# Optimization experiments

Measured on AMD Instinct MI355X. Metric: run time of the kernel, lower is better.

The kernel has to match this reference:

```python
import jax, jax.numpy as jnp
import numpy as np

B, T, I, H, O = 32, 128, 256, 512, 10


def setup_inputs() -> dict:
    key = jax.random.key(0)
    ks = jax.random.split(key, 16)
    s = 1.0 / np.sqrt(H)
    si = 1.0 / np.sqrt(I)
    inp = {
        "x": jax.random.normal(ks[0], (B, T, I), jnp.float32),
        # LSTM params (gate order: i, f, g, o)
        "Wih": jax.random.uniform(ks[1], (4 * H, I), jnp.float32, -si, si),
        "Whh": jax.random.uniform(ks[2], (4 * H, H), jnp.float32, -s, s),
        "b_lstm": jax.random.uniform(ks[3], (4 * H,), jnp.float32, -s, s),
        # readout dense
        "Wd": jax.random.uniform(ks[4], (O, H), jnp.float32, -s, s),
        "bd": jnp.zeros((O,), jnp.float32),
        # synthetic gradient MLP: H -> 512 -> 256 -> 128 -> H
        "Ws1": jax.random.uniform(ks[5], (512, H), jnp.float32, -s, s),
        "bs1": jnp.zeros((512,), jnp.float32),
        "Ws2": jax.random.uniform(ks[6], (256, 512), jnp.float32, -1.0 / np.sqrt(512), 1.0 / np.sqrt(512)),
        "bs2": jnp.zeros((256,), jnp.float32),
        "Ws3": jax.random.uniform(ks[7], (128, 256), jnp.float32, -1.0 / np.sqrt(256), 1.0 / np.sqrt(256)),
        "bs3": jnp.zeros((128,), jnp.float32),
        "Ws4": jax.random.uniform(ks[8], (H, 128), jnp.float32, -1.0 / np.sqrt(128), 1.0 / np.sqrt(128)),
        "bs4": jnp.zeros((H,), jnp.float32),
    }
    return inp


def reference(x, Wih, Whh, b_lstm, Wd, bd, Ws1, bs1, Ws2, bs2, Ws3, bs3, Ws4, bs4):
    # batch_first: [B,T,I] -> [T,B,I]
    xs = jnp.swapaxes(x, 0, 1)
    b, hid = x.shape[0], Whh.shape[1]

    h0 = jnp.zeros((b, hid), x.dtype)
    c0 = jnp.zeros((b, hid), x.dtype)
    # e-prop eligibility vectors: one row per (gate in {i,f,g}) x hidden unit
    ev_x0 = jnp.zeros((b, 3 * hid, Wih.shape[1]), x.dtype)
    ev_h0 = jnp.zeros((b, 3 * hid, hid), x.dtype)
    ev_b0 = jnp.zeros((b, 3 * hid, 1), x.dtype)

    def step(carry, xt):
        h, c, ev_x, ev_h, ev_b = carry
        gates = xt @ Wih.T + h @ Whh.T + b_lstm  # [B,4H]
        gi, gf, gg, go = jnp.split(gates, 4, axis=1)
        i = jax.nn.sigmoid(gi)
        f = jax.nn.sigmoid(gf)
        g = jnp.tanh(gg)
        o = jax.nn.sigmoid(go)
        # d(c_t)/d(pre-activation) for cell-affecting gates i, f, g  -> [B,3H]
        d = jnp.concatenate([g * i * (1.0 - i),
                             c * f * (1.0 - f),
                             i * (1.0 - g * g)], axis=1)
        f3 = jnp.concatenate([f, f, f], axis=1)  # forget-gate decay, tiled per gate
        # eligibility trace outer-product updates (the memory-bound core)
        ev_x_n = ev_x * f3[:, :, None] + d[:, :, None] * xt[:, None, :]
        ev_h_n = ev_h * f3[:, :, None] + d[:, :, None] * h[:, None, :]
        ev_b_n = ev_b * f3[:, :, None] + d[:, :, None]
        c_n = f * c + i * g
        h_n = o * jnp.tanh(c_n)
        return (h_n, c_n, ev_x_n, ev_h_n, ev_b_n), h_n

    (hT, cT, ev_x, ev_h, ev_b), hs = jax.lax.scan(step, (h0, c0, ev_x0, ev_h0, ev_b0), xs)

    last = hs[-1]  # [B,H]
    # synthetic gradient MLP on last hidden state
    z = jax.nn.relu(last @ Ws1.T + bs1)
    z = jax.nn.relu(z @ Ws2.T + bs2)
    z = jax.nn.relu(z @ Ws3.T + bs3)
    synth_grad = z @ Ws4.T + bs4  # [B,H]
    # readout on last hidden state (single_output=True)
    predictions = last @ Wd.T + bd  # [B,O]
    return (predictions, synth_grad, ev_x, ev_h, ev_b)
```

## Files before the change

kernel.cpp:

```cpp
#include <hip/hip_runtime.h>


typedef __attribute__((ext_vector_type(8))) short short8;
typedef __attribute__((ext_vector_type(4))) float f32x4;
typedef __attribute__((ext_vector_type(4))) unsigned u32x4;

#define DEV static __device__ __forceinline__

DEV unsigned f2bf(float x) {
  union { float f; unsigned u; } v; v.f = x;
  return (v.u + 0x7fffu + ((v.u >> 16) & 1u)) >> 16;
}
DEV float bf2f(unsigned b) {
  union { float f; unsigned u; } v; v.u = b << 16;
  return v.f;
}
struct HiLo { unsigned hi, lo; };
DEV HiLo packpair(float a, float b) {
  unsigned ha = f2bf(a), hb = f2bf(b);
  unsigned la = f2bf(a - bf2f(ha)), lb = f2bf(b - bf2f(hb));
  HiLo r; r.hi = ha | (hb << 16); r.lo = la | (lb << 16);
  return r;
}

#define SENT 0x7F7F7F7Fu

__global__ __launch_bounds__(512, 1) void lstm_rec(
    const float* __restrict__ Whh,
    const float* __restrict__ XW,
    unsigned* __restrict__ Hp,
    float* __restrict__ Hf,
    float* __restrict__ dh,
    float* __restrict__ fh)
{
  const int wg   = blockIdx.x;
  const int tid  = threadIdx.x;
  const int lane = tid & 63;
  const int wave = tid >> 6;
  const int tM   = wave & 1;
  const int tN   = wave >> 1;

  __shared__ __align__(16) unsigned Ldh[32 * 256];
  __shared__ float gl[32][68];

  const int cc = lane & 15;
  const int kb = lane >> 4;

  const int rloc  = tN * 16 + cc;
  const int jglob = (rloc >> 4) * 512 + wg * 16 + (rloc & 15);
  short8 whi[16], wlo[16];
#pragma unroll
  for (int s = 0; s < 16; ++s) {
    const float* wp = Whh + (size_t)jglob * 512 + s * 32 + kb * 8;
    f32x4 w0 = *(const f32x4*)wp;
    f32x4 w1 = *(const f32x4*)(wp + 4);
    short8 hi, lo;
#pragma unroll
    for (int j = 0; j < 4; ++j) {
      unsigned h0 = f2bf(w0[j]);
      hi[j] = (short)h0;  lo[j] = (short)f2bf(w0[j] - bf2f(h0));
      unsigned h1 = f2bf(w1[j]);
      hi[4 + j] = (short)h1;  lo[4 + j] = (short)f2bf(w1[j] - bf2f(h1));
    }
    whi[s] = hi; wlo[s] = lo;
  }

  const int bA = tM * 16 + cc;
  const int mz = bA & 7;
  const unsigned rbase = (unsigned)(bA * 256 + ((kb ^ (mz & 3)) << 2) + ((mz >> 2) << 4));

  const int beW = lane >> 1;
  const int swz = beW & 7;

  const int be = tid >> 4;
  const int jo = tid & 15;
  const int jh = wg * 16 + jo;
  float c_reg = 0.f;

  for (int t = 0; t < 128; ++t) {
    const float* xwp = XW + (size_t)t * 65536 + (size_t)be * 2048 + wg * 16 + jo;
    float xwi = xwp[0], xwf = xwp[512], xwg = xwp[1024], xwo = xwp[1536];

    if (t > 0) {
      const unsigned* sp = Hp + ((size_t)t * 32 + wave * 4) * 256 + lane * 4;
      u32x4 h0, h1, h2, h3;
      for (;;) {
#define SLICE_LOAD(dst, addr)                                          \
        asm volatile("global_load_dwordx4 %0, %1, off sc0 sc1"         \
                     : "=&v"(dst) : "v"(addr) : "memory")
        SLICE_LOAD(h0, sp);
        SLICE_LOAD(h1, sp + 256);
        SLICE_LOAD(h2, sp + 512);
        SLICE_LOAD(h3, sp + 768);
#undef SLICE_LOAD
        asm volatile("s_waitcnt vmcnt(0)" ::: "memory");
        __builtin_amdgcn_sched_barrier(0);
        unsigned bad = 0u;
#define CHK(v) bad |= (unsigned)((v[0] == SENT) | (v[1] == SENT) | \
                                 (v[2] == SENT) | (v[3] == SENT))
        CHK(h0); CHK(h1); CHK(h2); CHK(h3);
#undef CHK
        if (!__any((int)bad)) break;
        __builtin_amdgcn_s_sleep(1);
      }
      __builtin_amdgcn_sched_barrier(0);

      const int c0 = wave * 8 + (lane & 1);
      const unsigned wb = (unsigned)(beW * 256);
      *(u32x4*)&Ldh[wb + (((c0 + 0) ^ swz) << 2)] = h0;
      *(u32x4*)&Ldh[wb + (((c0 + 2) ^ swz) << 2)] = h1;
      *(u32x4*)&Ldh[wb + (((c0 + 4) ^ swz) << 2)] = h2;
      *(u32x4*)&Ldh[wb + (((c0 + 6) ^ swz) << 2)] = h3;
    }
    __syncthreads();

    f32x4 acc;
    {
      f32x4 a0 = {0.f, 0.f, 0.f, 0.f}, a1 = a0;
      if (t > 0) {
#pragma unroll
        for (int s = 0; s < 16; ++s) {
          const unsigned idx = rbase ^ (unsigned)(s << 4);
          short8 ah = __builtin_bit_cast(short8, *(const u32x4*)&Ldh[idx]);
          a0 = __builtin_amdgcn_mfma_f32_16x16x32_bf16(ah, whi[s], a0, 0, 0, 0);
          a1 = __builtin_amdgcn_mfma_f32_16x16x32_bf16(ah, wlo[s], a1, 0, 0, 0);
        }
      }
      acc = a0 + a1;
    }
#pragma unroll
    for (int r = 0; r < 4; ++r)
      gl[tM * 16 + kb * 4 + r][tN * 16 + cc] = acc[r];
    __syncthreads();

    {
      float pi = xwi + gl[be][jo];
      float pf = xwf + gl[be][16 + jo];
      float pg = xwg + gl[be][32 + jo];
      float po = xwo + gl[be][48 + jo];
      float ig = 1.f / (1.f + expf(-pi));
      float fg = 1.f / (1.f + expf(-pf));
      float gg = tanhf(pg);
      float og = 1.f / (1.f + expf(-po));
      float di = gg * ig * (1.f - ig);
      float df = c_reg * fg * (1.f - fg);
      float dg = ig * (1.f - gg * gg);
      c_reg = fg * c_reg + ig * gg;
      float hn = og * tanhf(c_reg);

      unsigned hh = f2bf(hn);
      unsigned hh_nb = (unsigned)__shfl_xor((int)hh, 1);
      if (!(tid & 1)) {
        unsigned stv = hh | (hh_nb << 16);
        size_t sa = ((size_t)(t + 1) * 32 + wg) * 256 + (tid >> 1);
        __hip_atomic_store(&Hp[sa], stv, __ATOMIC_RELAXED, __HIP_MEMORY_SCOPE_AGENT);
      }

      Hf[(size_t)(t + 1) * 16384 + (size_t)be * 512 + jh] = hn;
      size_t db = (size_t)t * 49152 + (size_t)be * 1536 + jh;
      dh[db] = di; dh[db + 512] = df; dh[db + 1024] = dg;
      fh[(size_t)t * 16384 + (size_t)be * 512 + jh] = fg;
    }
  }
}

__global__ __launch_bounds__(256) void suffix_pre(
    const float* __restrict__ fh, float* __restrict__ Cp)
{
  const int g = blockIdx.x * 256 + threadIdx.x;
  const int k = g >> 14, bjh = g & 16383;
  const int b = bjh >> 9, jh = bjh & 511;
  float P = 1.f;
  for (int t = k * 32; t < k * 32 + 32; ++t)
    P *= fh[(size_t)t * 16384 + (size_t)b * 512 + jh];
  Cp[g] = P;
}

__global__ __launch_bounds__(256) void suffix_main(
    float* __restrict__ dh, const float* __restrict__ fh,
    const float* __restrict__ Cp, float* __restrict__ Sp)
{
  const int g = blockIdx.x * 256 + threadIdx.x;
  const int k = g >> 14, bjh = g & 16383;
  const int b = bjh >> 9, jh = bjh & 511;
  float F = 1.f;
  for (int k2 = k + 1; k2 < 4; ++k2) F *= Cp[(k2 << 14) | bjh];
  float s0 = 0.f, s1 = 0.f, s2 = 0.f;
  for (int t = k * 32 + 31; t >= k * 32; --t) {
    size_t db = (size_t)t * 49152 + (size_t)b * 1536 + jh;
    float a0 = dh[db] * F, a1 = dh[db + 512] * F, a2 = dh[db + 1024] * F;
    dh[db] = a0; dh[db + 512] = a1; dh[db + 1024] = a2;
    s0 += a0; s1 += a1; s2 += a2;
    F *= fh[(size_t)t * 16384 + (size_t)b * 512 + jh];
  }
  size_t sb = (size_t)(k * 32 + b) * 1536 + jh;
  Sp[sb] = s0; Sp[sb + 512] = s1; Sp[sb + 1024] = s2;
}

__global__ __launch_bounds__(256) void evb_reduce(
    const float* __restrict__ Sp, float* __restrict__ evb)
{
  const int g = blockIdx.x * 256 + threadIdx.x;
  evb[g] = Sp[g] + Sp[49152 + g] + Sp[98304 + g] + Sp[147456 + g];
}

__global__ __launch_bounds__(256, 2) void gemm_bf16s(
    const float* __restrict__ A, const float* __restrict__ B,
    float* __restrict__ C, const float* __restrict__ bias,
    int M, int N, int K,
    long long sAm, long long sAk, long long aBatch,
    long long sBn, long long sBk, long long bBatch,
    long long sCm1, long long sCm2, int M1, long long cBatch)
{
  __shared__ __align__(16) unsigned Ahi[128 * 20], Alo[128 * 20];
  __shared__ __align__(16) unsigned Bhi[128 * 20], Blo[128 * 20];

  const int tid  = threadIdx.x;
  const int lane = tid & 63;
  const int wave = tid >> 6;
  const int wm   = wave >> 1;
  const int wn   = wave & 1;
  const int cc   = lane & 15;
  const int kb   = lane >> 4;
  const long long z = blockIdx.z;
  const float* Ab = A + z * aBatch;
  const float* Bb = B + z * bBatch;
  const int m0 = blockIdx.y * 128, n0 = blockIdx.x * 128;

  f32x4 acc[4][4];
#pragma unroll
  for (int i = 0; i < 4; ++i)
#pragma unroll
    for (int j = 0; j < 4; ++j) acc[i][j] = (f32x4){0.f, 0.f, 0.f, 0.f};

  for (int k0 = 0; k0 < K; k0 += 32) {
    if (sAk == 1) {
      const int r = tid >> 1, half = tid & 1;
      const float* s = Ab + (long long)(m0 + r) * sAm + (k0 + half * 16);
      f32x4 v0 = *(const f32x4*)s;
      f32x4 v1 = *(const f32x4*)(s + 4);
      f32x4 v2 = *(const f32x4*)(s + 8);
      f32x4 v3 = *(const f32x4*)(s + 12);
      u32x4 h0, h1, l0, l1;
      HiLo p;
      p = packpair(v0[0], v0[1]); h0[0] = p.hi; l0[0] = p.lo;
      p = packpair(v0[2], v0[3]); h0[1] = p.hi; l0[1] = p.lo;
      p = packpair(v1[0], v1[1]); h0[2] = p.hi; l0[2] = p.lo;
      p = packpair(v1[2], v1[3]); h0[3] = p.hi; l0[3] = p.lo;
      p = packpair(v2[0], v2[1]); h1[0] = p.hi; l1[0] = p.lo;
      p = packpair(v2[2], v2[3]); h1[1] = p.hi; l1[1] = p.lo;
      p = packpair(v3[0], v3[1]); h1[2] = p.hi; l1[2] = p.lo;
      p = packpair(v3[2], v3[3]); h1[3] = p.hi; l1[3] = p.lo;
      const int o = r * 20 + half * 8;
      *(u32x4*)&Ahi[o] = h0;  *(u32x4*)&Ahi[o + 4] = h1;
      *(u32x4*)&Alo[o] = l0;  *(u32x4*)&Alo[o + 4] = l1;
    } else {
#pragma unroll
      for (int it = 0; it < 2; ++it) {
        const int kp = tid >> 4;
        const int mr = (tid & 15) * 4 + it * 64;
        const float* s0 = Ab + (long long)(k0 + 2 * kp) * sAk + (m0 + mr);
        f32x4 va = *(const f32x4*)s0;
        f32x4 vb = *(const f32x4*)(s0 + sAk);
#pragma unroll
        for (int q = 0; q < 4; ++q) {
          HiLo p = packpair(va[q], vb[q]);
          Ahi[(mr + q) * 20 + kp] = p.hi;
          Alo[(mr + q) * 20 + kp] = p.lo;
        }
      }
    }
    if (sBk == 1) {
      const int r = tid >> 1, half = tid & 1;
      const float* s = Bb + (long long)(n0 + r) * sBn + (k0 + half * 16);
      f32x4 v0 = *(const f32x4*)s;
      f32x4 v1 = *(const f32x4*)(s + 4);
      f32x4 v2 = *(const f32x4*)(s + 8);
      f32x4 v3 = *(const f32x4*)(s + 12);
      u32x4 h0, h1, l0, l1;
      HiLo p;
      p = packpair(v0[0], v0[1]); h0[0] = p.hi; l0[0] = p.lo;
      p = packpair(v0[2], v0[3]); h0[1] = p.hi; l0[1] = p.lo;
      p = packpair(v1[0], v1[1]); h0[2] = p.hi; l0[2] = p.lo;
      p = packpair(v1[2], v1[3]); h0[3] = p.hi; l0[3] = p.lo;
      p = packpair(v2[0], v2[1]); h1[0] = p.hi; l1[0] = p.lo;
      p = packpair(v2[2], v2[3]); h1[1] = p.hi; l1[1] = p.lo;
      p = packpair(v3[0], v3[1]); h1[2] = p.hi; l1[2] = p.lo;
      p = packpair(v3[2], v3[3]); h1[3] = p.hi; l1[3] = p.lo;
      const int o = r * 20 + half * 8;
      *(u32x4*)&Bhi[o] = h0;  *(u32x4*)&Bhi[o + 4] = h1;
      *(u32x4*)&Blo[o] = l0;  *(u32x4*)&Blo[o + 4] = l1;
    } else {
#pragma unroll
      for (int it = 0; it < 2; ++it) {
        const int kp = tid >> 4;
        const int nr = (tid & 15) * 4 + it * 64;
        const float* s0 = Bb + (long long)(k0 + 2 * kp) * sBk + (n0 + nr);
        f32x4 va = *(const f32x4*)s0;
        f32x4 vb = *(const f32x4*)(s0 + sBk);
#pragma unroll
        for (int q = 0; q < 4; ++q) {
          HiLo p = packpair(va[q], vb[q]);
          Bhi[(nr + q) * 20 + kp] = p.hi;
          Blo[(nr + q) * 20 + kp] = p.lo;
        }
      }
    }
    __syncthreads();

    short8 ah[4], al[4], bh[4], bl[4];
#pragma unroll
    for (int mi = 0; mi < 4; ++mi) {
      const int row = wm * 64 + mi * 16 + cc;
      ah[mi] = __builtin_bit_cast(short8, *(const u32x4*)&Ahi[row * 20 + kb * 4]);
      al[mi] = __builtin_bit_cast(short8, *(const u32x4*)&Alo[row * 20 + kb * 4]);
    }
#pragma unroll
    for (int ni = 0; ni < 4; ++ni) {
      const int row = wn * 64 + ni * 16 + cc;
      bh[ni] = __builtin_bit_cast(short8, *(const u32x4*)&Bhi[row * 20 + kb * 4]);
      bl[ni] = __builtin_bit_cast(short8, *(const u32x4*)&Blo[row * 20 + kb * 4]);
    }
#pragma unroll
    for (int mi = 0; mi < 4; ++mi)
#pragma unroll
      for (int ni = 0; ni < 4; ++ni) {
        acc[mi][ni] = __builtin_amdgcn_mfma_f32_16x16x32_bf16(ah[mi], bh[ni], acc[mi][ni], 0, 0, 0);
        acc[mi][ni] = __builtin_amdgcn_mfma_f32_16x16x32_bf16(ah[mi], bl[ni], acc[mi][ni], 0, 0, 0);
        acc[mi][ni] = __builtin_amdgcn_mfma_f32_16x16x32_bf16(al[mi], bh[ni], acc[mi][ni], 0, 0, 0);
      }
    __syncthreads();
  }

#pragma unroll
  for (int ni = 0; ni < 4; ++ni) {
    const int ng = n0 + wn * 64 + ni * 16 + cc;
    const float bv = bias ? bias[ng] : 0.f;
#pragma unroll
    for (int mi = 0; mi < 4; ++mi) {
#pragma unroll
      for (int r = 0; r < 4; ++r) {
        const int mg = m0 + wm * 64 + mi * 16 + kb * 4 + r;
        const long long crow = z * cBatch + (long long)(mg % M1) * sCm1 +
                               (long long)(mg / M1) * sCm2;
        C[crow + ng] = acc[mi][ni][r] + bv;
      }
    }
  }
}

template <int BM, int BN, int TM, int TN>
__global__ __launch_bounds__(256) void gemm_f32(
    const float* __restrict__ A, const float* __restrict__ B,
    float* __restrict__ C, const float* __restrict__ bias,
    int M, int N, int K,
    long long sAm, long long sAk, long long aBatch,
    long long sBn, long long sBk, long long bBatch,
    long long sCm1, long long sCm2, int M1, long long cBatch,
    int relu)
{
  constexpr int BK = 16;
  __shared__ float As[BK][BM + 4];
  __shared__ float Bs[BK][BN + 4];
  const int tid = threadIdx.x;
  const long long z = blockIdx.z;
  const float* Ab = A + z * aBatch;
  const float* Bb = B + z * bBatch;
  const int m0 = blockIdx.y * BM, n0 = blockIdx.x * BN;
  constexpr int tn_cnt = BN / TN;
  const int tm0 = (tid / tn_cnt) * TM;
  const int tn0 = (tid % tn_cnt) * TN;

  float acc[TM][TN];
#pragma unroll
  for (int i = 0; i < TM; ++i)
#pragma unroll
    for (int j = 0; j < TN; ++j) acc[i][j] = 0.f;

  for (int k0 = 0; k0 < K; k0 += BK) {
    if (sAk == 1) {
      for (int m = tid >> 2; m < BM; m += 64) {
        const int kq = (tid & 3) * 4;
        f32x4 v = {0.f, 0.f, 0.f, 0.f};
        if (m0 + m < M) v = *(const f32x4*)(Ab + (long long)(m0 + m) * sAm + (k0 + kq));
        As[kq + 0][m] = v[0]; As[kq + 1][m] = v[1];
        As[kq + 2][m] = v[2]; As[kq + 3][m] = v[3];
      }
    } else {
      constexpr int mq_cnt = BM / 4;
      for (int kk = tid / mq_cnt; kk < BK; kk += 256 / mq_cnt) {
        const int mq = (tid % mq_cnt) * 4;
        f32x4 v = {0.f, 0.f, 0.f, 0.f};
        if (m0 + mq < M) v = *(const f32x4*)(Ab + (long long)(k0 + kk) * sAk + (m0 + mq));
        *(f32x4*)&As[kk][mq] = v;
      }
    }
    if (sBk == 1) {
      for (int n = tid >> 2; n < BN; n += 64) {
        const int kq = (tid & 3) * 4;
        f32x4 v = {0.f, 0.f, 0.f, 0.f};
        if (n0 + n < N) v = *(const f32x4*)(Bb + (long long)(n0 + n) * sBn + (k0 + kq));
        Bs[kq + 0][n] = v[0]; Bs[kq + 1][n] = v[1];
        Bs[kq + 2][n] = v[2]; Bs[kq + 3][n] = v[3];
      }
    } else {
      constexpr int nq_cnt = BN / 4;
      for (int kk = tid / nq_cnt; kk < BK; kk += 256 / nq_cnt) {
        const int nq = (tid % nq_cnt) * 4;
        f32x4 v = {0.f, 0.f, 0.f, 0.f};
        if (n0 + nq < N) v = *(const f32x4*)(Bb + (long long)(k0 + kk) * sBk + (n0 + nq));
        *(f32x4*)&Bs[kk][nq] = v;
      }
    }
    __syncthreads();

#pragma unroll
    for (int kk = 0; kk < BK; ++kk) {
      float a[TM], bb[TN];
#pragma unroll
      for (int i = 0; i < TM; ++i) a[i] = As[kk][tm0 + i];
#pragma unroll
      for (int j = 0; j < TN; ++j) bb[j] = Bs[kk][tn0 + j];
#pragma unroll
      for (int i = 0; i < TM; ++i)
#pragma unroll
        for (int j = 0; j < TN; ++j) acc[i][j] += a[i] * bb[j];
    }
    __syncthreads();
  }

#pragma unroll
  for (int i = 0; i < TM; ++i) {
    const int mg = m0 + tm0 + i;
    if (mg >= M) continue;
    const long long crow = z * cBatch + (long long)(mg % M1) * sCm1 +
                           (long long)(mg / M1) * sCm2;
#pragma unroll
    for (int j = 0; j < TN; ++j) {
      const int ng = n0 + tn0 + j;
      if (ng >= N) continue;
      float v = acc[i][j];
      if (bias) v += bias[ng];
      if (relu) v = fmaxf(v, 0.f);
      C[crow + ng] = v;
    }
  }
}

extern "C" void kernel_launch(void* const* d_in, const int* in_sizes, int n_in,
                              void* d_out, int out_size, void* d_ws, size_t ws_size,
                              hipStream_t stream) {
  const float* x   = (const float*)d_in[0];
  const float* Wih = (const float*)d_in[1];
  const float* Whh = (const float*)d_in[2];
  const float* bl  = (const float*)d_in[3];
  const float* Wd  = (const float*)d_in[4];
  const float* bd  = (const float*)d_in[5];
  const float* Ws1 = (const float*)d_in[6];
  const float* bs1 = (const float*)d_in[7];
  const float* Ws2 = (const float*)d_in[8];
  const float* bs2 = (const float*)d_in[9];
  const float* Ws3 = (const float*)d_in[10];
  const float* bs3 = (const float*)d_in[11];
  const float* Ws4 = (const float*)d_in[12];
  const float* bs4 = (const float*)d_in[13];

  float* out = (float*)d_out;
  float* ws  = (float*)d_ws;

  const long long OP = 0, OS = 320, OEX = 16704, OEH = 12599616, OEB = 37765440;

  float* XW = out + OEH;
  float* fh = out + OEH + 8388608;
  unsigned* Hp = (unsigned*)(out + OEH + 10485760);
  float* Cp = out + OEH + 12599296;
  float* Sp = out + OEH + 12664832;

  float* dh = ws;
  float* Hf = ws + 6291456;
  float* z1 = ws + 8404992;
  float* z2 = ws + 8421376;
  float* z3 = ws + 8429568;

  hipMemsetAsync(Hp, 0x7F, 129ull * 32 * 256 * sizeof(unsigned), stream);
  hipMemsetAsync(Hf, 0, 16384 * sizeof(float), stream);

  dim3 blk(256);

  gemm_bf16s<<<dim3(16, 32, 1), blk, 0, stream>>>(
      x, Wih, XW, bl, 4096, 2048, 256,
      256, 1, 0,
      256, 1, 0,
      65536, 2048, 128, 0);

  lstm_rec<<<dim3(32), dim3(512), 0, stream>>>(Whh, XW, Hp, Hf, dh, fh);

  suffix_pre<<<dim3(256), blk, 0, stream>>>(fh, Cp);
  suffix_main<<<dim3(256), blk, 0, stream>>>(dh, fh, Cp, Sp);
  evb_reduce<<<dim3(192), blk, 0, stream>>>(Sp, out + OEB);

  const float* hlast = Hf + 2097152;
  gemm_f32<32, 32, 2, 2><<<dim3(16, 1, 1), blk, 0, stream>>>(
      hlast, Ws1, z1, bs1, 32, 512, 512, 512, 1, 0, 512, 1, 0, 512, 0, 32, 0, 1);
  gemm_f32<32, 32, 2, 2><<<dim3(8, 1, 1), blk, 0, stream>>>(
      z1, Ws2, z2, bs2, 32, 256, 512, 512, 1, 0, 512, 1, 0, 256, 0, 32, 0, 1);
  gemm_f32<32, 32, 2, 2><<<dim3(4, 1, 1), blk, 0, stream>>>(
      z2, Ws3, z3, bs3, 32, 128, 256, 256, 1, 0, 256, 1, 0, 128, 0, 32, 0, 1);
  gemm_f32<32, 32, 2, 2><<<dim3(16, 1, 1), blk, 0, stream>>>(
      z3, Ws4, out + OS, bs4, 32, 512, 128, 128, 1, 0, 128, 1, 0, 512, 0, 32, 0, 0);
  gemm_f32<32, 32, 2, 2><<<dim3(1, 1, 1), blk, 0, stream>>>(
      hlast, Wd, out + OP, bd, 32, 10, 512, 512, 1, 0, 512, 1, 0, 10, 0, 32, 0, 0);

  gemm_bf16s<<<dim3(2, 12, 32), blk, 0, stream>>>(
      dh, x, out + OEX, nullptr, 1536, 256, 128,
      1, 49152, 1536,
      1, 256, 32768,
      256, 0, 1536, 393216);

  gemm_bf16s<<<dim3(4, 12, 32), blk, 0, stream>>>(
      dh, Hf, out + OEH, nullptr, 1536, 512, 128,
      1, 49152, 1536,
      1, 16384, 512,
      512, 0, 1536, 786432);
}
```

Measured before the change: 633.6 us.

## Drop bf16 split-precision recurrence, halve LSTM grid, merge suffix kernels

```diff
diff --git a/kernel.cpp b/kernel.cpp
--- a/kernel.cpp
+++ b/kernel.cpp
@@ -25,7 +25,7 @@
 
 #define SENT 0x7F7F7F7Fu
 
-__global__ __launch_bounds__(512, 1) void lstm_rec(
+__global__ __launch_bounds__(1024) void lstm_rec(
     const float* __restrict__ Whh,
     const float* __restrict__ XW,
     unsigned* __restrict__ Hp,
@@ -41,76 +41,70 @@
   const int tN   = wave >> 1;
 
   __shared__ __align__(16) unsigned Ldh[32 * 256];
-  __shared__ float gl[32][68];
+  __shared__ float gl[32][132];
 
   const int cc = lane & 15;
   const int kb = lane >> 4;
 
   const int rloc  = tN * 16 + cc;
-  const int jglob = (rloc >> 4) * 512 + wg * 16 + (rloc & 15);
-  short8 whi[16], wlo[16];
+  const int jglob = (rloc >> 5) * 512 + wg * 32 + (rloc & 31);
+  short8 whi[16];
 #pragma unroll
   for (int s = 0; s < 16; ++s) {
     const float* wp = Whh + (size_t)jglob * 512 + s * 32 + kb * 8;
     f32x4 w0 = *(const f32x4*)wp;
     f32x4 w1 = *(const f32x4*)(wp + 4);
-    short8 hi, lo;
+    short8 hi;
 #pragma unroll
     for (int j = 0; j < 4; ++j) {
-      unsigned h0 = f2bf(w0[j]);
-      hi[j] = (short)h0;  lo[j] = (short)f2bf(w0[j] - bf2f(h0));
-      unsigned h1 = f2bf(w1[j]);
-      hi[4 + j] = (short)h1;  lo[4 + j] = (short)f2bf(w1[j] - bf2f(h1));
-    }
-    whi[s] = hi; wlo[s] = lo;
+      hi[j]     = (short)f2bf(w0[j]);
+      hi[4 + j] = (short)f2bf(w1[j]);
+    }
+    whi[s] = hi;
   }
 
   const int bA = tM * 16 + cc;
   const int mz = bA & 7;
   const unsigned rbase = (unsigned)(bA * 256 + ((kb ^ (mz & 3)) << 2) + ((mz >> 2) << 4));
 
-  const int beW = lane >> 1;
-  const int swz = beW & 7;
-
-  const int be = tid >> 4;
-  const int jo = tid & 15;
-  const int jh = wg * 16 + jo;
+  const int beW  = lane >> 1;
+  const int half = lane & 1;
+  const int swz  = beW & 7;
+  const int C0   = wave * 4 + half * 2;
+
+  const int be = tid >> 5;
+  const int jo = tid & 31;
+  const int jh = wg * 32 + jo;
   float c_reg = 0.f;
 
   for (int t = 0; t < 128; ++t) {
-    const float* xwp = XW + (size_t)t * 65536 + (size_t)be * 2048 + wg * 16 + jo;
+    const float* xwp = XW + (size_t)t * 65536 + (size_t)be * 2048 + wg * 32 + jo;
     float xwi = xwp[0], xwf = xwp[512], xwg = xwp[1024], xwo = xwp[1536];
 
     if (t > 0) {
-      const unsigned* sp = Hp + ((size_t)t * 32 + wave * 4) * 256 + lane * 4;
-      u32x4 h0, h1, h2, h3;
+      const unsigned* sp = Hp + ((size_t)t * 16 + wave) * 512 + lane * 8;
+      u32x4 h0, h1;
       for (;;) {
 #define SLICE_LOAD(dst, addr)                                          \
         asm volatile("global_load_dwordx4 %0, %1, off sc0 sc1"         \
                      : "=&v"(dst) : "v"(addr) : "memory")
         SLICE_LOAD(h0, sp);
-        SLICE_LOAD(h1, sp + 256);
-        SLICE_LOAD(h2, sp + 512);
-        SLICE_LOAD(h3, sp + 768);
+        SLICE_LOAD(h1, sp + 4);
 #undef SLICE_LOAD
         asm volatile("s_waitcnt vmcnt(0)" ::: "memory");
         __builtin_amdgcn_sched_barrier(0);
-        unsigned bad = 0u;
-#define CHK(v) bad |= (unsigned)((v[0] == SENT) | (v[1] == SENT) | \
-                                 (v[2] == SENT) | (v[3] == SENT))
-        CHK(h0); CHK(h1); CHK(h2); CHK(h3);
-#undef CHK
+        unsigned bad = (unsigned)((h0[0] == SENT) | (h0[1] == SENT) |
+                                  (h0[2] == SENT) | (h0[3] == SENT) |
+                                  (h1[0] == SENT) | (h1[1] == SENT) |
+                                  (h1[2] == SENT) | (h1[3] == SENT));
         if (!__any((int)bad)) break;
         __builtin_amdgcn_s_sleep(1);
       }
       __builtin_amdgcn_sched_barrier(0);
 
-      const int c0 = wave * 8 + (lane & 1);
       const unsigned wb = (unsigned)(beW * 256);
-      *(u32x4*)&Ldh[wb + (((c0 + 0) ^ swz) << 2)] = h0;
-      *(u32x4*)&Ldh[wb + (((c0 + 2) ^ swz) << 2)] = h1;
-      *(u32x4*)&Ldh[wb + (((c0 + 4) ^ swz) << 2)] = h2;
-      *(u32x4*)&Ldh[wb + (((c0 + 6) ^ swz) << 2)] = h3;
+      *(u32x4*)&Ldh[wb + (((C0 + 0) ^ swz) << 2)] = h0;
+      *(u32x4*)&Ldh[wb + (((C0 + 1) ^ swz) << 2)] = h1;
     }
     __syncthreads();
 
@@ -119,11 +113,13 @@
       f32x4 a0 = {0.f, 0.f, 0.f, 0.f}, a1 = a0;
       if (t > 0) {
 #pragma unroll
-        for (int s = 0; s < 16; ++s) {
-          const unsigned idx = rbase ^ (unsigned)(s << 4);
-          short8 ah = __builtin_bit_cast(short8, *(const u32x4*)&Ldh[idx]);
-          a0 = __builtin_amdgcn_mfma_f32_16x16x32_bf16(ah, whi[s], a0, 0, 0, 0);
-          a1 = __builtin_amdgcn_mfma_f32_16x16x32_bf16(ah, wlo[s], a1, 0, 0, 0);
+        for (int s = 0; s < 16; s += 2) {
+          const unsigned i0 = rbase ^ (unsigned)(s << 4);
+          const unsigned i1 = rbase ^ (unsigned)((s + 1) << 4);
+          short8 ah0 = __builtin_bit_cast(short8, *(const u32x4*)&Ldh[i0]);
+          short8 ah1 = __builtin_bit_cast(short8, *(const u32x4*)&Ldh[i1]);
+          a0 = __builtin_amdgcn_mfma_f32_16x16x32_bf16(ah0, whi[s],     a0, 0, 0, 0);
+          a1 = __builtin_amdgcn_mfma_f32_16x16x32_bf16(ah1, whi[s + 1], a1, 0, 0, 0);
         }
       }
       acc = a0 + a1;
@@ -135,9 +131,9 @@
 
     {
       float pi = xwi + gl[be][jo];
-      float pf = xwf + gl[be][16 + jo];
-      float pg = xwg + gl[be][32 + jo];
-      float po = xwo + gl[be][48 + jo];
+      float pf = xwf + gl[be][32 + jo];
+      float pg = xwg + gl[be][64 + jo];
+      float po = xwo + gl[be][96 + jo];
       float ig = 1.f / (1.f + expf(-pi));
       float fg = 1.f / (1.f + expf(-pf));
       float gg = tanhf(pg);
@@ -150,9 +146,9 @@
 
       unsigned hh = f2bf(hn);
       unsigned hh_nb = (unsigned)__shfl_xor((int)hh, 1);
-      if (!(tid & 1)) {
+      if (!(jo & 1)) {
         unsigned stv = hh | (hh_nb << 16);
-        size_t sa = ((size_t)(t + 1) * 32 + wg) * 256 + (tid >> 1);
+        size_t sa = ((size_t)(t + 1) * 16 + wg) * 512 + be * 16 + (jo >> 1);
         __hip_atomic_store(&Hp[sa], stv, __ATOMIC_RELAXED, __HIP_MEMORY_SCOPE_AGENT);
       }
 
@@ -164,44 +160,22 @@
   }
 }
 
-__global__ __launch_bounds__(256) void suffix_pre(
-    const float* __restrict__ fh, float* __restrict__ Cp)
+__global__ __launch_bounds__(256) void suffix_A(
+    float* __restrict__ dh, const float* __restrict__ fh,
+    float* __restrict__ evb)
 {
   const int g = blockIdx.x * 256 + threadIdx.x;
-  const int k = g >> 14, bjh = g & 16383;
-  const int b = bjh >> 9, jh = bjh & 511;
-  float P = 1.f;
-  for (int t = k * 32; t < k * 32 + 32; ++t)
-    P *= fh[(size_t)t * 16384 + (size_t)b * 512 + jh];
-  Cp[g] = P;
-}
-
-__global__ __launch_bounds__(256) void suffix_main(
-    float* __restrict__ dh, const float* __restrict__ fh,
-    const float* __restrict__ Cp, float* __restrict__ Sp)
-{
-  const int g = blockIdx.x * 256 + threadIdx.x;
-  const int k = g >> 14, bjh = g & 16383;
-  const int b = bjh >> 9, jh = bjh & 511;
-  float F = 1.f;
-  for (int k2 = k + 1; k2 < 4; ++k2) F *= Cp[(k2 << 14) | bjh];
-  float s0 = 0.f, s1 = 0.f, s2 = 0.f;
-  for (int t = k * 32 + 31; t >= k * 32; --t) {
+  const int b = g >> 9, jh = g & 511;
+  float F = 1.f, s0 = 0.f, s1 = 0.f, s2 = 0.f;
+  for (int t = 127; t >= 0; --t) {
     size_t db = (size_t)t * 49152 + (size_t)b * 1536 + jh;
     float a0 = dh[db] * F, a1 = dh[db + 512] * F, a2 = dh[db + 1024] * F;
     dh[db] = a0; dh[db + 512] = a1; dh[db + 1024] = a2;
     s0 += a0; s1 += a1; s2 += a2;
     F *= fh[(size_t)t * 16384 + (size_t)b * 512 + jh];
   }
-  size_t sb = (size_t)(k * 32 + b) * 1536 + jh;
-  Sp[sb] = s0; Sp[sb + 512] = s1; Sp[sb + 1024] = s2;
-}
-
-__global__ __launch_bounds__(256) void evb_reduce(
-    const float* __restrict__ Sp, float* __restrict__ evb)
-{
-  const int g = blockIdx.x * 256 + threadIdx.x;
-  evb[g] = Sp[g] + Sp[49152 + g] + Sp[98304 + g] + Sp[147456 + g];
+  size_t eb = (size_t)b * 1536 + jh;
+  evb[eb] = s0; evb[eb + 512] = s1; evb[eb + 1024] = s2;
 }
 
 __global__ __launch_bounds__(256, 2) void gemm_bf16s(
@@ -473,8 +447,6 @@
   float* XW = out + OEH;
   float* fh = out + OEH + 8388608;
   unsigned* Hp = (unsigned*)(out + OEH + 10485760);
-  float* Cp = out + OEH + 12599296;
-  float* Sp = out + OEH + 12664832;
 
   float* dh = ws;
   float* Hf = ws + 6291456;
@@ -482,7 +454,7 @@
   float* z2 = ws + 8421376;
   float* z3 = ws + 8429568;
 
-  hipMemsetAsync(Hp, 0x7F, 129ull * 32 * 256 * sizeof(unsigned), stream);
+  hipMemsetAsync(Hp, 0x7F, 129ull * 16 * 512 * sizeof(unsigned), stream);
   hipMemsetAsync(Hf, 0, 16384 * sizeof(float), stream);
 
   dim3 blk(256);
@@ -493,11 +465,9 @@
       256, 1, 0,
       65536, 2048, 128, 0);
 
-  lstm_rec<<<dim3(32), dim3(512), 0, stream>>>(Whh, XW, Hp, Hf, dh, fh);
-
-  suffix_pre<<<dim3(256), blk, 0, stream>>>(fh, Cp);
-  suffix_main<<<dim3(256), blk, 0, stream>>>(dh, fh, Cp, Sp);
-  evb_reduce<<<dim3(192), blk, 0, stream>>>(Sp, out + OEB);
+  lstm_rec<<<dim3(16), dim3(1024), 0, stream>>>(Whh, XW, Hp, Hf, dh, fh);
+
+  suffix_A<<<dim3(64), blk, 0, stream>>>(dh, fh, out + OEB);
 
   const float* hlast = Hf + 2097152;
   gemm_f32<32, 32, 2, 2><<<dim3(16, 1, 1), blk, 0, stream>>>(
```

Result: slower. 775.9 us (+22.5%).
